# Optimization experiments

Measured on AMD Instinct MI355X. Metric: run time of the kernel, lower is better.

Reference implementation:

```python
import jax, jax.numpy as jnp
import numpy as np

B, T, V, D = 2048, 32, 1024, 256


def setup_inputs() -> dict:
    key = jax.random.key(0)
    k1, k2 = jax.random.split(key)
    input = jax.random.normal(k1, (B, T, D), dtype=jnp.float32)
    codebook = jax.random.normal(k2, (T, V, D), dtype=jnp.float32)
    return {"input": input, "codebook": codebook}


def reference(input, codebook):
    # input: [B, T, D]; codebook: [T, V, D]
    x = jnp.moveaxis(input, 1, 0)  # [T, B, D]
    # Squared euclidean distances; argmin is invariant to the sqrt in cdist.
    x2 = jnp.sum(x * x, axis=-1)[..., None]            # [T, B, 1]
    c2 = jnp.sum(codebook * codebook, axis=-1)[:, None, :]  # [T, 1, V]
    xc = jnp.einsum('tbd,tvd->tbv', x, codebook)       # [T, B, V]
    d2 = x2 - 2.0 * xc + c2                            # [T, B, V]
    idxes_ = jnp.argmin(d2, axis=-1)                   # [T, B]
    idxes = idxes_.T                                   # [B, T]
    # Direct per-token gather: embed[b, t] = codebook[t, idxes[b, t]]
    embed_ = codebook[jnp.arange(T)[:, None], idxes_]  # [T, B, D]
    embed = jnp.moveaxis(embed_, 0, 1)                 # [B, T, D]
    return embed, idxes
```

## Files before the change

### kernel.cpp

```cpp
#include <hip/hip_runtime.h>
#include <hip/hip_bf16.h>


#define B_ 2048
#define T_ 32
#define V_ 1024
#define D_ 256
#define BT 64
#define VT 128
#define NVT 8
#define CAND_MAX 1024
#define MARGIN 8.0f

typedef __attribute__((ext_vector_type(8))) short short8;
typedef __attribute__((ext_vector_type(4))) float f32x4;

__device__ __forceinline__ unsigned short f2bf(float f) {
    unsigned u = __builtin_bit_cast(unsigned, f);
    unsigned r = u + 0x7FFFu + ((u >> 16) & 1u);
    return (unsigned short)(r >> 16);
}

__device__ __forceinline__ short8 pack8(float4 a, float4 b) {
    short8 r;
    r[0] = (short)f2bf(a.x); r[1] = (short)f2bf(a.y);
    r[2] = (short)f2bf(a.z); r[3] = (short)f2bf(a.w);
    r[4] = (short)f2bf(b.x); r[5] = (short)f2bf(b.y);
    r[6] = (short)f2bf(b.z); r[7] = (short)f2bf(b.w);
    return r;
}

__global__ void prep_kernel(const float* __restrict__ cb, float* __restrict__ c2,
                            unsigned short* __restrict__ cbb) {
    const int wave = threadIdx.x >> 6, lane = threadIdx.x & 63;
    const int row = blockIdx.x * 4 + wave;
    const float4 v4 = *(const float4*)(cb + (size_t)row * D_ + lane * 4);
    float s = v4.x * v4.x + v4.y * v4.y + v4.z * v4.z + v4.w * v4.w;
    #pragma unroll
    for (int off = 32; off; off >>= 1) s += __shfl_down(s, off, 64);
    if (lane == 0) c2[row] = s;

    ushort4 b4;
    b4.x = f2bf(v4.x); b4.y = f2bf(v4.y); b4.z = f2bf(v4.z); b4.w = f2bf(v4.w);
    *(ushort4*)(cbb + (size_t)row * D_ + lane * 4) = b4;
}

__global__ void c2_kernel(const float* __restrict__ cb, float* __restrict__ c2) {
    const int row = blockIdx.x * 4 + (threadIdx.x >> 6);
    const int lane = threadIdx.x & 63;
    const float4 v = ((const float4*)(cb + (size_t)row * D_))[lane];
    float s = v.x * v.x + v.y * v.y + v.z * v.z + v.w * v.w;
    #pragma unroll
    for (int off = 32; off; off >>= 1) s += __shfl_down(s, off, 64);
    if (lane == 0) c2[row] = s;
}

__global__ __launch_bounds__(256, 4)
void vq_kernel(const float* __restrict__ x, const float* __restrict__ cb,
               const float* __restrict__ c2, const unsigned short* __restrict__ cbb,
               float* __restrict__ out, int use_bf) {
    const int t  = blockIdx.x;
    const int b0 = blockIdx.y * BT;

    __shared__ short8 A_lds[BT * 32];
    __shared__ float  minPart[BT * 2];
    __shared__ unsigned long long result[BT];
    __shared__ unsigned s_cand[CAND_MAX];
    __shared__ unsigned s_cnt;

    const int tid = threadIdx.x;
    const int wave = tid >> 6, lane = tid & 63;
    const int wm = wave & 1, wn = wave >> 1;
    const int q = lane >> 4, ln = lane & 15;

    if (tid < BT) result[tid] = ~0ULL;
    if (tid < BT * 2) minPart[tid] = 3.4e38f;
    if (tid == 0) s_cnt = 0;

    #pragma unroll
    for (int i = 0; i < 8; ++i) {
        int gid = i * 256 + tid, r = gid >> 5, g = gid & 31;
        const float4* src = (const float4*)(x + (((size_t)(b0 + r)) * T_ + t) * D_ + g * 8);
        A_lds[r * 32 + (g ^ (r & 15))] = pack8(src[0], src[1]);
    }

    const unsigned short* bb = cbb + ((size_t)t * V_ + wn * 64 + ln) * D_ + q * 8;
    const float*          fb = cb  + ((size_t)t * V_ + wn * 64 + ln) * D_ + q * 8;

    auto loadB = [&](int vt, int kc, short8 (&dst)[4]) {
        #pragma unroll
        for (int nt = 0; nt < 4; ++nt) {
            const int off = (vt * VT + nt * 16) * D_ + kc * 32;
            if (use_bf) {
                dst[nt] = *(const short8*)(bb + off);
            } else {
                const float4* s = (const float4*)(fb + off);
                dst[nt] = pack8(s[0], s[1]);
            }
        }
    };

    short8 bufs[2][4];
    loadB(0, 0, bufs[0]);
    __syncthreads();

    const int abase = (wm * 32 + ln) * 32;

    #pragma unroll
    for (int vt = 0; vt < NVT; ++vt) {
        f32x4 acc[2][4];
        #pragma unroll
        for (int mt = 0; mt < 2; ++mt)
            #pragma unroll
            for (int nt = 0; nt < 4; ++nt) acc[mt][nt] = (f32x4){0.f, 0.f, 0.f, 0.f};

        #pragma unroll
        for (int kc = 0; kc < 8; ++kc) {
            if (!(vt == NVT - 1 && kc == 7)) {
                const int s1 = vt * 8 + kc + 1;
                loadB(s1 >> 3, s1 & 7, bufs[(kc + 1) & 1]);
            }
            short8 af[2];
            af[0] = A_lds[abase + ((kc * 4 + q) ^ ln)];
            af[1] = A_lds[abase + 512 + ((kc * 4 + q) ^ ln)];
            #pragma unroll
            for (int mt = 0; mt < 2; ++mt)
                #pragma unroll
                for (int nt = 0; nt < 4; ++nt)
                    acc[mt][nt] = __builtin_amdgcn_mfma_f32_16x16x32_bf16(
                        af[mt], bufs[kc & 1][nt], acc[mt][nt], 0, 0, 0);
        }

        const float* c2p = c2 + t * V_ + vt * VT + wn * 64 + ln;
        float cc[4];
        #pragma unroll
        for (int nt = 0; nt < 4; ++nt) cc[nt] = c2p[nt * 16];

        #pragma unroll
        for (int mt = 0; mt < 2; ++mt)
            #pragma unroll
            for (int i = 0; i < 4; ++i) {
                float mn = 3.4e38f;
                #pragma unroll
                for (int nt = 0; nt < 4; ++nt)
                    mn = fminf(mn, fmaf(-2.0f, acc[mt][nt][i], cc[nt]));
                mn = fminf(mn, __shfl_xor(mn, 1, 64));
                mn = fminf(mn, __shfl_xor(mn, 2, 64));
                mn = fminf(mn, __shfl_xor(mn, 4, 64));
                mn = fminf(mn, __shfl_xor(mn, 8, 64));
                if (ln == 0) {
                    int r = wm * 32 + mt * 16 + q * 4 + i;
                    minPart[r * 2 + wn] = fminf(minPart[r * 2 + wn], mn);
                }
            }
        __syncthreads();

        #pragma unroll
        for (int mt = 0; mt < 2; ++mt)
            #pragma unroll
            for (int i = 0; i < 4; ++i) {
                const int r = wm * 32 + mt * 16 + q * 4 + i;
                float2 mp = *(const float2*)&minPart[r * 2];
                float thr = fminf(mp.x, mp.y) + MARGIN;
                #pragma unroll
                for (int nt = 0; nt < 4; ++nt) {
                    float s = fmaf(-2.0f, acc[mt][nt][i], cc[nt]);
                    const bool pred = (s < thr);
                    unsigned long long m = __ballot(pred);
                    if (m) {
                        const int first = __ffsll((unsigned long long)m) - 1;
                        unsigned base = 0;
                        if (lane == first) base = atomicAdd(&s_cnt, (unsigned)__popcll(m));
                        base = __shfl(base, first, 64);
                        if (pred) {
                            unsigned pos = base + (unsigned)__popcll(m & ((1ull << lane) - 1ull));
                            if (pos < CAND_MAX) {
                                int v = vt * VT + wn * 64 + nt * 16 + ln;
                                s_cand[pos] = (unsigned)((r << 10) | v);
                            }
                        }
                    }
                }
            }
    }

    __syncthreads();
    const unsigned ncand = min(s_cnt, (unsigned)CAND_MAX);
    const int grp = tid >> 4, l16 = tid & 15;
    for (unsigned ci = grp; ci < ncand; ci += 16) {
        const unsigned e = s_cand[ci];
        const int row = e >> 10, v = e & 1023;
        const float* xr = x + (((size_t)(b0 + row)) * T_ + t) * D_ + l16 * 16;
        const float* cr = cb + ((size_t)t * V_ + v) * D_ + l16 * 16;
        float dot = 0.f;
        #pragma unroll
        for (int j = 0; j < 4; ++j) {
            float4 a = *(const float4*)(xr + j * 4);
            float4 b = *(const float4*)(cr + j * 4);
            dot = fmaf(a.x, b.x, dot); dot = fmaf(a.y, b.y, dot);
            dot = fmaf(a.z, b.z, dot); dot = fmaf(a.w, b.w, dot);
        }
        dot += __shfl_xor(dot, 1, 64);
        dot += __shfl_xor(dot, 2, 64);
        dot += __shfl_xor(dot, 4, 64);
        dot += __shfl_xor(dot, 8, 64);
        if (l16 == 0) {
            float sc = fmaf(-2.0f, dot, c2[t * V_ + v]);
            unsigned u = __builtin_bit_cast(unsigned, sc);
            u = (u & 0x80000000u) ? ~u : (u | 0x80000000u);
            atomicMin(&result[row], ((unsigned long long)u << 32) | (unsigned)v);
        }
    }
    __syncthreads();

    if (tid < BT)
        out[(size_t)B_ * T_ * D_ + (size_t)(b0 + tid) * T_ + t] =
            (float)(int)(result[tid] & 1023u);

    #pragma unroll
    for (int i = 0; i < 16; ++i) {
        const int row = wave * 16 + i;
        const int idx = (int)(result[row] & 1023u);
        const float4 src = *(const float4*)(cb + ((size_t)t * V_ + idx) * D_ + lane * 4);
        *(float4*)(out + (((size_t)(b0 + row)) * T_ + t) * D_ + lane * 4) = src;
    }
}

extern "C" void kernel_launch(void* const* d_in, const int* in_sizes, int n_in,
                              void* d_out, int out_size, void* d_ws, size_t ws_size,
                              hipStream_t stream) {
    const float* x  = (const float*)d_in[0];
    const float* cb = (const float*)d_in[1];
    float* out = (float*)d_out;
    float* c2  = (float*)d_ws;
    unsigned short* cbb = (unsigned short*)((char*)d_ws + 131072);
    const size_t NEED = 131072 + (size_t)T_ * V_ * D_ * 2;
    const int use_bf = (ws_size >= NEED) ? 1 : 0;

    if (use_bf) prep_kernel<<<dim3(T_ * V_ / 4), 256, 0, stream>>>(cb, c2, cbb);
    else        c2_kernel<<<dim3(T_ * V_ / 4), 256, 0, stream>>>(cb, c2);
    vq_kernel<<<dim3(T_, B_ / BT), 256, 0, stream>>>(x, cb, c2, cbb, out, use_bf);
}
```

Before: 307.2 us.

## Widen per-wave V tile, use per-row candidate lists, template bf16 path

Each wave now covers all 64 rows against its own 64-column slice of a 256-wide V tile (4x4 MFMA tiles), so the V loop runs 4 iterations instead of 8 and each A fragment feeds more MFMAs. The global candidate list with ballot-based compaction is replaced by per-row candidate lists of at most 32 entries. Each row's x slice is loaded once during rescoring and the best candidate is reduced in registers rather than with 64-bit atomics. A row whose list overflows falls back to rescoring all 1024 codes. The use_bf flag becomes a template parameter, and launch bounds drop to 3 blocks per CU because the larger accumulator set needs more registers.

```diff
diff --git a/kernel.cpp b/kernel.cpp
--- a/kernel.cpp
+++ b/kernel.cpp
@@ -7,9 +7,9 @@
 #define V_ 1024
 #define D_ 256
 #define BT 64
-#define VT 128
-#define NVT 8
-#define CAND_MAX 1024
+#define VTILE 256
+#define NVT 4
+#define CAP 32
 #define MARGIN 8.0f
 
 typedef __attribute__((ext_vector_type(8))) short short8;
@@ -55,27 +55,26 @@
     if (lane == 0) c2[row] = s;
 }
 
-__global__ __launch_bounds__(256, 4)
+template<int USE_BF>
+__global__ __launch_bounds__(256, 3)
 void vq_kernel(const float* __restrict__ x, const float* __restrict__ cb,
                const float* __restrict__ c2, const unsigned short* __restrict__ cbb,
-               float* __restrict__ out, int use_bf) {
+               float* __restrict__ out) {
     const int t  = blockIdx.x;
     const int b0 = blockIdx.y * BT;
 
     __shared__ short8 A_lds[BT * 32];
-    __shared__ float  minPart[BT * 2];
-    __shared__ unsigned long long result[BT];
-    __shared__ unsigned s_cand[CAND_MAX];
-    __shared__ unsigned s_cnt;
+    __shared__ float  minPart4[BT][4];
+    __shared__ unsigned rowCnt[BT];
+    __shared__ unsigned short rowCand[BT * CAP];
+    __shared__ unsigned short rowIdx[BT];
 
     const int tid = threadIdx.x;
-    const int wave = tid >> 6, lane = tid & 63;
-    const int wm = wave & 1, wn = wave >> 1;
+    const int w = tid >> 6, lane = tid & 63;
     const int q = lane >> 4, ln = lane & 15;
 
-    if (tid < BT) result[tid] = ~0ULL;
-    if (tid < BT * 2) minPart[tid] = 3.4e38f;
-    if (tid == 0) s_cnt = 0;
+    if (tid < BT) rowCnt[tid] = 0;
+    ((float*)minPart4)[tid] = 3.4e38f;
 
     #pragma unroll
     for (int i = 0; i < 8; ++i) {
@@ -84,14 +83,14 @@
         A_lds[r * 32 + (g ^ (r & 15))] = pack8(src[0], src[1]);
     }
 
-    const unsigned short* bb = cbb + ((size_t)t * V_ + wn * 64 + ln) * D_ + q * 8;
-    const float*          fb = cb  + ((size_t)t * V_ + wn * 64 + ln) * D_ + q * 8;
+    const unsigned short* bb = cbb + ((size_t)t * V_ + w * 64 + ln) * D_ + q * 8;
+    const float*          fb = cb  + ((size_t)t * V_ + w * 64 + ln) * D_ + q * 8;
 
     auto loadB = [&](int vt, int kc, short8 (&dst)[4]) {
         #pragma unroll
         for (int nt = 0; nt < 4; ++nt) {
-            const int off = (vt * VT + nt * 16) * D_ + kc * 32;
-            if (use_bf) {
+            const int off = (vt * VTILE + nt * 16) * D_ + kc * 32;
+            if constexpr (USE_BF) {
                 dst[nt] = *(const short8*)(bb + off);
             } else {
                 const float4* s = (const float4*)(fb + off);
@@ -100,44 +99,42 @@
         }
     };
 
-    short8 bufs[2][4];
-    loadB(0, 0, bufs[0]);
+    short8 bufs0[4], bufs1[4];
+    loadB(0, 0, bufs0);
     __syncthreads();
 
-    const int abase = (wm * 32 + ln) * 32;
-
-    #pragma unroll
     for (int vt = 0; vt < NVT; ++vt) {
-        f32x4 acc[2][4];
-        #pragma unroll
-        for (int mt = 0; mt < 2; ++mt)
+        f32x4 acc[4][4];
+        #pragma unroll
+        for (int mt = 0; mt < 4; ++mt)
             #pragma unroll
             for (int nt = 0; nt < 4; ++nt) acc[mt][nt] = (f32x4){0.f, 0.f, 0.f, 0.f};
 
         #pragma unroll
         for (int kc = 0; kc < 8; ++kc) {
             if (!(vt == NVT - 1 && kc == 7)) {
-                const int s1 = vt * 8 + kc + 1;
-                loadB(s1 >> 3, s1 & 7, bufs[(kc + 1) & 1]);
-            }
-            short8 af[2];
-            af[0] = A_lds[abase + ((kc * 4 + q) ^ ln)];
-            af[1] = A_lds[abase + 512 + ((kc * 4 + q) ^ ln)];
-            #pragma unroll
-            for (int mt = 0; mt < 2; ++mt)
+                if (kc & 1) loadB(vt + (kc == 7), (kc + 1) & 7, bufs0);
+                else        loadB(vt,             kc + 1,       bufs1);
+            }
+            short8 af[4];
+            #pragma unroll
+            for (int mt = 0; mt < 4; ++mt)
+                af[mt] = A_lds[(mt * 16 + ln) * 32 + ((kc * 4 + q) ^ ln)];
+            #pragma unroll
+            for (int mt = 0; mt < 4; ++mt)
                 #pragma unroll
                 for (int nt = 0; nt < 4; ++nt)
                     acc[mt][nt] = __builtin_amdgcn_mfma_f32_16x16x32_bf16(
-                        af[mt], bufs[kc & 1][nt], acc[mt][nt], 0, 0, 0);
+                        af[mt], (kc & 1) ? bufs1[nt] : bufs0[nt], acc[mt][nt], 0, 0, 0);
         }
 
-        const float* c2p = c2 + t * V_ + vt * VT + wn * 64 + ln;
+        const float* c2p = c2 + t * V_ + vt * VTILE + w * 64 + ln;
         float cc[4];
         #pragma unroll
         for (int nt = 0; nt < 4; ++nt) cc[nt] = c2p[nt * 16];
 
         #pragma unroll
-        for (int mt = 0; mt < 2; ++mt)
+        for (int mt = 0; mt < 4; ++mt)
             #pragma unroll
             for (int i = 0; i < 4; ++i) {
                 float mn = 3.4e38f;
@@ -149,78 +146,79 @@
                 mn = fminf(mn, __shfl_xor(mn, 4, 64));
                 mn = fminf(mn, __shfl_xor(mn, 8, 64));
                 if (ln == 0) {
-                    int r = wm * 32 + mt * 16 + q * 4 + i;
-                    minPart[r * 2 + wn] = fminf(minPart[r * 2 + wn], mn);
+                    const int r = mt * 16 + q * 4 + i;
+                    minPart4[r][w] = fminf(minPart4[r][w], mn);
                 }
             }
         __syncthreads();
 
         #pragma unroll
-        for (int mt = 0; mt < 2; ++mt)
+        for (int mt = 0; mt < 4; ++mt)
             #pragma unroll
             for (int i = 0; i < 4; ++i) {
-                const int r = wm * 32 + mt * 16 + q * 4 + i;
-                float2 mp = *(const float2*)&minPart[r * 2];
-                float thr = fminf(mp.x, mp.y) + MARGIN;
+                const int r = mt * 16 + q * 4 + i;
+                const float4 mp = *(const float4*)minPart4[r];
+                const float thr = fminf(fminf(mp.x, mp.y), fminf(mp.z, mp.w)) + MARGIN;
                 #pragma unroll
                 for (int nt = 0; nt < 4; ++nt) {
                     float s = fmaf(-2.0f, acc[mt][nt][i], cc[nt]);
-                    const bool pred = (s < thr);
-                    unsigned long long m = __ballot(pred);
-                    if (m) {
-                        const int first = __ffsll((unsigned long long)m) - 1;
-                        unsigned base = 0;
-                        if (lane == first) base = atomicAdd(&s_cnt, (unsigned)__popcll(m));
-                        base = __shfl(base, first, 64);
-                        if (pred) {
-                            unsigned pos = base + (unsigned)__popcll(m & ((1ull << lane) - 1ull));
-                            if (pos < CAND_MAX) {
-                                int v = vt * VT + wn * 64 + nt * 16 + ln;
-                                s_cand[pos] = (unsigned)((r << 10) | v);
-                            }
-                        }
+                    if (s < thr) {
+                        unsigned pos = atomicAdd(&rowCnt[r], 1u);
+                        if (pos < CAP)
+                            rowCand[r * CAP + pos] =
+                                (unsigned short)(vt * VTILE + w * 64 + nt * 16 + ln);
                     }
                 }
             }
     }
 
     __syncthreads();
-    const unsigned ncand = min(s_cnt, (unsigned)CAND_MAX);
     const int grp = tid >> 4, l16 = tid & 15;
-    for (unsigned ci = grp; ci < ncand; ci += 16) {
-        const unsigned e = s_cand[ci];
-        const int row = e >> 10, v = e & 1023;
-        const float* xr = x + (((size_t)(b0 + row)) * T_ + t) * D_ + l16 * 16;
-        const float* cr = cb + ((size_t)t * V_ + v) * D_ + l16 * 16;
-        float dot = 0.f;
-        #pragma unroll
-        for (int j = 0; j < 4; ++j) {
-            float4 a = *(const float4*)(xr + j * 4);
-            float4 b = *(const float4*)(cr + j * 4);
-            dot = fmaf(a.x, b.x, dot); dot = fmaf(a.y, b.y, dot);
-            dot = fmaf(a.z, b.z, dot); dot = fmaf(a.w, b.w, dot);
-        }
-        dot += __shfl_xor(dot, 1, 64);
-        dot += __shfl_xor(dot, 2, 64);
-        dot += __shfl_xor(dot, 4, 64);
-        dot += __shfl_xor(dot, 8, 64);
-        if (l16 == 0) {
+    #pragma unroll
+    for (int j = 0; j < 4; ++j) {
+        const int r = grp * 4 + j;
+        const float* xp = x + (((size_t)(b0 + r)) * T_ + t) * D_ + l16 * 16;
+        float4 xr[4];
+        #pragma unroll
+        for (int k = 0; k < 4; ++k) xr[k] = ((const float4*)xp)[k];
+
+        const unsigned cnt = rowCnt[r];
+        unsigned long long best = ~0ULL;
+        auto score_v = [&](int v) {
+            const float* cr = cb + ((size_t)t * V_ + v) * D_ + l16 * 16;
+            float dot = 0.f;
+            #pragma unroll
+            for (int k = 0; k < 4; ++k) {
+                float4 b = ((const float4*)cr)[k];
+                dot = fmaf(xr[k].x, b.x, dot); dot = fmaf(xr[k].y, b.y, dot);
+                dot = fmaf(xr[k].z, b.z, dot); dot = fmaf(xr[k].w, b.w, dot);
+            }
+            dot += __shfl_xor(dot, 1, 64);
+            dot += __shfl_xor(dot, 2, 64);
+            dot += __shfl_xor(dot, 4, 64);
+            dot += __shfl_xor(dot, 8, 64);
             float sc = fmaf(-2.0f, dot, c2[t * V_ + v]);
             unsigned u = __builtin_bit_cast(unsigned, sc);
             u = (u & 0x80000000u) ? ~u : (u | 0x80000000u);
-            atomicMin(&result[row], ((unsigned long long)u << 32) | (unsigned)v);
+            unsigned long long e = ((unsigned long long)u << 32) | (unsigned)v;
+            if (e < best) best = e;
+        };
+        if (cnt <= CAP) {
+            for (unsigned c = 0; c < cnt; ++c) score_v((int)rowCand[r * CAP + c]);
+        } else {
+            for (int v = 0; v < V_; ++v) score_v(v);
         }
+        if (l16 == 0) rowIdx[r] = (unsigned short)(best & 1023u);
     }
     __syncthreads();
 
     if (tid < BT)
-        out[(size_t)B_ * T_ * D_ + (size_t)(b0 + tid) * T_ + t] =
-            (float)(int)(result[tid] & 1023u);
+        out[(size_t)B_ * T_ * D_ + (size_t)(b0 + tid) * T_ + t] = (float)rowIdx[tid];
 
     #pragma unroll
     for (int i = 0; i < 16; ++i) {
-        const int row = wave * 16 + i;
-        const int idx = (int)(result[row] & 1023u);
+        const int row = w * 16 + i;
+        const int idx = (int)rowIdx[row];
         const float4 src = *(const float4*)(cb + ((size_t)t * V_ + idx) * D_ + lane * 4);
         *(float4*)(out + (((size_t)(b0 + row)) * T_ + t) * D_ + lane * 4) = src;
     }
@@ -237,7 +235,11 @@
     const size_t NEED = 131072 + (size_t)T_ * V_ * D_ * 2;
     const int use_bf = (ws_size >= NEED) ? 1 : 0;
 
-    if (use_bf) prep_kernel<<<dim3(T_ * V_ / 4), 256, 0, stream>>>(cb, c2, cbb);
-    else        c2_kernel<<<dim3(T_ * V_ / 4), 256, 0, stream>>>(cb, c2);
-    vq_kernel<<<dim3(T_, B_ / BT), 256, 0, stream>>>(x, cb, c2, cbb, out, use_bf);
-}
+    if (use_bf) {
+        prep_kernel<<<dim3(T_ * V_ / 4), 256, 0, stream>>>(cb, c2, cbb);
+        vq_kernel<1><<<dim3(T_, B_ / BT), 256, 0, stream>>>(x, cb, c2, cbb, out);
+    } else {
+        c2_kernel<<<dim3(T_ * V_ / 4), 256, 0, stream>>>(cb, c2);
+        vq_kernel<0><<<dim3(T_, B_ / BT), 256, 0, stream>>>(x, cb, c2, cbb, out);
+    }
+}
```

New measurement: 281.4 us. -8.4%, faster.
